# Kernel tuning notes

Measured on AMD Instinct MI355X. Metric: run time of the kernel, lower is better.

Reference implementation:

```python
import jax, jax.numpy as jnp
import numpy as np

B, L, W = 512, 16, 256


def setup_inputs() -> dict:
    key = jax.random.key(0)
    k = jax.random.split(key, 9)
    f32 = jnp.float32
    # spin configuration in {-1, +1}
    x = jax.random.randint(k[0], (B, L, L), 0, 2).astype(f32) * 2.0 - 1.0
    s = 1.0 / np.sqrt(W)
    W_ih = jax.random.normal(k[1], (3 * W, 2), f32) * s      # GRUCell input weights
    W_hh = jax.random.normal(k[2], (3 * W, W), f32) * s      # GRUCell hidden weights
    b_ih = jax.random.normal(k[3], (3 * W,), f32) * s
    b_hh = jax.random.normal(k[4], (3 * W,), f32) * s
    W_fc = jax.random.normal(k[5], (2, W), f32) * s          # fc1
    b_fc = jax.random.normal(k[6], (2,), f32) * s
    W_hcat = jax.random.normal(k[7], (W, 2 * W), f32) * (1.0 / np.sqrt(2 * W))  # intermediate_h
    W_xcat = jax.random.normal(k[8], (1, 2), f32) * 0.5      # intermediate_x
    return dict(x=x, W_ih=W_ih, W_hh=W_hh, b_ih=b_ih, b_hh=b_hh,
                W_fc=W_fc, b_fc=b_fc, W_hcat=W_hcat, W_xcat=W_xcat)


def _log_prob(x, W_ih, W_hh, b_ih, b_hh, W_fc, b_fc, W_hcat, W_xcat):
    Bsz, Ln, _ = x.shape
    Wd = W_hh.shape[1]
    mask = (1.0 + x) * 0.5                      # (1+x)/2
    Wh_l = W_hcat[:, :Wd]                       # acts on left-neighbor hidden (cat order: [left, up])
    Wh_u = W_hcat[:, Wd:]                       # acts on up-neighbor hidden

    def step(carry, xs):
        x_left, h_left = carry                  # [B], [B,W]
        x_cur, x_up, h_up, m = xs               # [B], [B], [B,W], [B]
        # intermediate_x(stack([x_left, x_up]))
        x_int = x_left * W_xcat[0, 0] + x_up * W_xcat[0, 1]
        # intermediate_h(cat([h_left, h_up]))
        h_int = h_left @ Wh_l.T + h_up @ Wh_u.T
        # embedded_x = [(x+1)/2, 1-(x+1)/2]
        p_up = (x_int + 1.0) * 0.5
        emb = jnp.stack([p_up, 1.0 - p_up], axis=1)   # [B,2]
        # torch.nn.GRUCell math (gate order: reset, update, new)
        gi = emb @ W_ih.T + b_ih
        gh = h_int @ W_hh.T + b_hh
        ir, iz, inn = jnp.split(gi, 3, axis=1)
        hr, hz, hn = jnp.split(gh, 3, axis=1)
        r = jax.nn.sigmoid(ir + hr)
        z = jax.nn.sigmoid(iz + hz)
        n = jnp.tanh(inn + r * hn)
        h_next = (1.0 - z) * n + z * h_int
        y = jax.nn.log_softmax(h_next @ W_fc.T + b_fc, axis=1)   # [B,2]
        lp = y[:, 0] * m + y[:, 1] * (1.0 - m)
        return (x_cur, h_next), (h_next, lp)

    h_prev = jnp.zeros((Ln, Bsz, Wd), x.dtype)  # hidden of row above, columns-major [L,B,W]
    x_prev = jnp.zeros((Ln, Bsz), x.dtype)      # spins of row above [L,B]
    lp_rows = []
    for i in range(Ln):                         # fixed small structural loop over rows
        x_row = x[:, i, :].T                    # [L,B]
        m_row = mask[:, i, :].T
        x_up, h_up = x_prev, h_prev
        if i % 2 == 1:                          # zigzag: odd rows scan right-to-left
            x_row, m_row = x_row[::-1], m_row[::-1]
            x_up, h_up = x_up[::-1], h_up[::-1]
        carry0 = (jnp.zeros((Bsz,), x.dtype), jnp.zeros((Bsz, Wd), x.dtype))
        _, (h_out, lp_out) = jax.lax.scan(step, carry0, (x_row, x_up, h_up, m_row))
        if i % 2 == 1:                          # restore grid (column) order
            h_out, lp_out = h_out[::-1], lp_out[::-1]
        lp_rows.append(lp_out)                  # [L,B]
        h_prev = h_out
        x_prev = x[:, i, :].T
    lp = jnp.transpose(jnp.stack(lp_rows, axis=0), (2, 0, 1))   # [B,L,L]
    lp = lp.at[:, 0, 0].set(1.0 - mask[:, 0, 0])                # first site overwrite
    return lp.sum(axis=(1, 2))


def reference(x, W_ih, W_hh, b_ih, b_hh, W_fc, b_fc, W_hcat, W_xcat):
    # z2 == 0 and reverse == False: log_prob(x) == _log_prob(x)
    return _log_prob(x, W_ih, W_hh, b_ih, b_hh, W_fc, b_fc, W_hcat, W_xcat)
```

## Files before the change

### kernel.cpp

```cpp
#include <hip/hip_runtime.h>
#include <math.h>

#define LL 16
#define WD 256
#define G3 768

#define OFF_A8  0
#define OFF_B8  32768
#define OFF_SRB 81920
#define OFF_SRA 82688
#define OFF_GA  82944
#define OFF_GBI 83712

__device__ __forceinline__ int sdot4(unsigned a, unsigned b, int acc) {
#if __has_builtin(__builtin_amdgcn_sdot4)
    return __builtin_amdgcn_sdot4((int)a, (int)b, acc, false);
#else
    int s = acc;
    #pragma unroll
    for (int r = 0; r < 4; ++r)
        s += (int)(signed char)(a >> (8 * r)) * (int)(signed char)(b >> (8 * r));
    return s;
#endif
}
__device__ __forceinline__ float fsig(float v) { return 1.f / (1.f + __expf(-v)); }
__device__ __forceinline__ float ftanh_(float v) {
    v = fminf(fmaxf(v, -15.f), 15.f);
    float e = __expf(-2.f * v);
    return (1.f - e) / (1.f + e);
}
__device__ __forceinline__ int clampi8(int q) {
    return q > 127 ? 127 : (q < -127 ? -127 : q);
}

__global__ __launch_bounds__(64)
void gru2d_prep1(const float* __restrict__ W_hh, const float* __restrict__ W_hcat,
                 float* __restrict__ ws) {
    int row = blockIdx.x, lane = threadIdx.x;
    float s = 0.f;
    if (row < 768) {
        for (int k = lane; k < 256; k += 64) s = fmaxf(s, fabsf(W_hh[row * 256 + k]));
    } else {
        int r = row - 768;
        for (int k = lane; k < 512; k += 64) s = fmaxf(s, fabsf(W_hcat[r * 512 + k]));
    }
    #pragma unroll
    for (int o = 32; o > 0; o >>= 1) s = fmaxf(s, __shfl_down(s, o));
    if (lane == 0) {
        float sc = (s > 0.f) ? s * (1.f / 127.f) : 1.f;
        if (row < 768) ws[OFF_SRB + row] = sc;
        else           ws[OFF_SRA + (row - 768)] = sc;
    }
}

__global__ __launch_bounds__(256)
void gru2d_prep2(const float* __restrict__ W_ih, const float* __restrict__ W_hh,
                 const float* __restrict__ b_ih, const float* __restrict__ W_hcat,
                 float* __restrict__ ws) {
    unsigned* __restrict__ wsu = (unsigned*)ws;
    int m = blockIdx.x * 256 + threadIdx.x;
    if (m < 32768) {
        int g4 = m >> 11, t = (m >> 2) & 511, r = m & 3;
        int j = g4 * 4 + r;
        int w = t & 255, ch = t >> 8;
        float inv = 1.f / ws[OFF_SRA + w];
        int base = w * 512 + ch * 256 + 4 * j;
        unsigned pk = 0;
        #pragma unroll
        for (int bb = 0; bb < 4; ++bb) {
            int qv = clampi8(__float2int_rn(W_hcat[base + bb] * inv));
            pk |= ((unsigned)(qv & 255)) << (8 * bb);
        }
        wsu[OFF_A8 + m] = pk;
    } else if (m < 81920) {
        int mm = m - 32768;
        int g4 = mm >> 11, t = (mm >> 2) & 511, rr = mm & 3;
        int ql = g4 * 4 + rr;
        int gate = ql >> 5, q = ql & 31;
        int v = t >> 6, l = t & 63;
        int wB_ = v * 32 + (l & 31), chB = l >> 5;
        int row = gate * 256 + wB_;
        float inv = 1.f / ws[OFF_SRB + row];
        int kb = row * 256 + chB * 128 + 4 * q;
        unsigned pk = 0;
        #pragma unroll
        for (int bb = 0; bb < 4; ++bb) {
            int qv = clampi8(__float2int_rn(W_hh[kb + bb] * inv));
            pk |= ((unsigned)(qv & 255)) << (8 * bb);
        }
        wsu[OFF_B8 + mm] = pk;
    } else if (m < 82688) {
        int e = m - 81920;
        float w0 = W_ih[2 * e], w1 = W_ih[2 * e + 1];
        ws[OFF_GA + e] = w0 - w1;
        ws[OFF_GBI + e] = w1 + b_ih[e];
    }
}

__global__ __launch_bounds__(512, 2)
void gru2d_main(const float* __restrict__ x, const float* __restrict__ b_hh,
                const float* __restrict__ W_fc, const float* __restrict__ b_fc,
                const float* __restrict__ W_xcat, const float* __restrict__ ws,
                float* __restrict__ out) {
    __shared__ __attribute__((aligned(16))) unsigned h8[2][64];
    __shared__ __attribute__((aligned(16))) unsigned hp8[2][LL][64];
    __shared__ float hs8[2][8];
    __shared__ float hps8[2][LL][8];
    __shared__ __attribute__((aligned(16))) float pA[2][2][256];
    __shared__ __attribute__((aligned(16))) float shint[2][256];
    __shared__ __attribute__((aligned(16))) unsigned hint8q[2][64];
    __shared__ float dqs[2][4];
    __shared__ float fcp[2][2][8];
    __shared__ float sx[2][256];

    const int tid = threadIdx.x;
    const int w = tid & 255;
    const int ch = tid >> 8;
    const int v = tid >> 6, l = tid & 63;
    const int lr = l & 31, sub = l >> 5;
    const int wB_ = (v << 5) + lr;
    const int b0 = blockIdx.x * 2;
    const unsigned* __restrict__ wsu = (const unsigned*)ws;

    unsigned wA8[64], wB8[96];
    #pragma unroll
    for (int g = 0; g < 16; ++g) {
        uint4 q = ((const uint4*)(wsu + OFF_A8))[g * 512 + tid];
        wA8[4*g] = q.x; wA8[4*g+1] = q.y; wA8[4*g+2] = q.z; wA8[4*g+3] = q.w;
    }
    #pragma unroll
    for (int g = 0; g < 24; ++g) {
        uint4 q = ((const uint4*)(wsu + OFF_B8))[g * 512 + tid];
        wB8[4*g] = q.x; wB8[4*g+1] = q.y; wB8[4*g+2] = q.z; wB8[4*g+3] = q.w;
    }

    const float ascale = ws[OFF_SRA + w];
    float bA[3], bBi[3], bbh[3], bsr[3];
    #pragma unroll
    for (int g = 0; g < 3; ++g) {
        bA[g]  = ws[OFF_GA + (g << 8) + wB_];
        bBi[g] = ws[OFF_GBI + (g << 8) + wB_];
        bbh[g] = b_hh[(g << 8) + wB_];
        bsr[g] = ws[OFF_SRB + (g << 8) + wB_];
    }
    const float wfc0 = W_fc[wB_], wfc1 = W_fc[256 + wB_];
    sx[ch][w] = x[(b0 + ch) * 256 + w];
    {
        unsigned* hp = (unsigned*)hp8;
        #pragma unroll
        for (int g = 0; g < 4; ++g) hp[g * 512 + tid] = 0u;
        if (tid < 256) ((float*)hps8)[tid] = 0.f;
    }
    const float xc0 = W_xcat[0], xc1 = W_xcat[1];
    const float bf0 = b_fc[0], bf1 = b_fc[1];
    float lp_acc = 0.f;
    __syncthreads();

    for (int i = 0; i < LL; ++i) {
        const int odd = i & 1;
        const int dir = odd ? -1 : 1;
        const int c0g = odd ? (LL - 1) : 0;
        for (int t = 0; t < LL; ++t) {
            const int col = c0g + dir * t;
            const int sidx = (i << 4) + t;

            #pragma unroll
            for (int g = 0; g < 16; ++g)
                asm volatile("" : "+v"(wA8[4*g]), "+v"(wA8[4*g+1]), "+v"(wA8[4*g+2]), "+v"(wA8[4*g+3]));
            #pragma unroll
            for (int g = 0; g < 24; ++g)
                asm volatile("" : "+v"(wB8[4*g]), "+v"(wB8[4*g+1]), "+v"(wB8[4*g+2]), "+v"(wB8[4*g+3]));

            {
                const uint4* Hb0;
                const uint4* Hb1;
                const float* sc0;
                const float* sc1;
                if (ch == 0) {
                    Hb0 = (const uint4*)h8[0];       Hb1 = (const uint4*)h8[1];
                    sc0 = hs8[0];                     sc1 = hs8[1];
                } else {
                    Hb0 = (const uint4*)hp8[0][col]; Hb1 = (const uint4*)hp8[1][col];
                    sc0 = hps8[0][col];               sc1 = hps8[1][col];
                }
                float fa0 = 0.f, fa1 = 0.f;
                if (!(ch == 0 && t == 0)) {
                    #pragma unroll
                    for (int c = 0; c < 8; ++c) {
                        uint4 u0a = Hb0[2*c], u0b = Hb0[2*c+1];
                        uint4 u1a = Hb1[2*c], u1b = Hb1[2*c+1];
                        int a0 = 0, a1 = 0;
                        const int kk = c << 3;
                        a0 = sdot4(wA8[kk],   u0a.x, a0); a0 = sdot4(wA8[kk+1], u0a.y, a0);
                        a0 = sdot4(wA8[kk+2], u0a.z, a0); a0 = sdot4(wA8[kk+3], u0a.w, a0);
                        a0 = sdot4(wA8[kk+4], u0b.x, a0); a0 = sdot4(wA8[kk+5], u0b.y, a0);
                        a0 = sdot4(wA8[kk+6], u0b.z, a0); a0 = sdot4(wA8[kk+7], u0b.w, a0);
                        a1 = sdot4(wA8[kk],   u1a.x, a1); a1 = sdot4(wA8[kk+1], u1a.y, a1);
                        a1 = sdot4(wA8[kk+2], u1a.z, a1); a1 = sdot4(wA8[kk+3], u1a.w, a1);
                        a1 = sdot4(wA8[kk+4], u1b.x, a1); a1 = sdot4(wA8[kk+5], u1b.y, a1);
                        a1 = sdot4(wA8[kk+6], u1b.z, a1); a1 = sdot4(wA8[kk+7], u1b.w, a1);
                        fa0 += (float)a0 * sc0[c];
                        fa1 += (float)a1 * sc1[c];
                    }
                    fa0 *= ascale;
                    fa1 *= ascale;
                }
                pA[ch][0][w] = fa0;
                pA[ch][1][w] = fa1;
            }
            __syncthreads();

            {
                float hi = pA[0][ch][w] + pA[1][ch][w];
                shint[ch][w] = hi;
                float am = fabsf(hi);
                #pragma unroll
                for (int o = 1; o < 64; o <<= 1) am = fmaxf(am, __shfl_xor(am, o));
                float qsc = 127.f / fmaxf(am, 1e-20f);
                int q = clampi8(__float2int_rn(hi * qsc));
                ((unsigned char*)hint8q)[(ch << 8) + w] = (unsigned char)(q & 255);
                if ((w & 63) == 0) dqs[ch][w >> 6] = am * (1.f / 127.f);

                if (w == 0 && sidx > 0) {
                    int ps = sidx - 1, pi2 = ps >> 4, pt2 = ps & 15;
                    int pcol = (pi2 & 1) ? (15 - pt2) : pt2;
                    float l0 = bf0, l1 = bf1;
                    #pragma unroll
                    for (int vv = 0; vv < 8; ++vv) { l0 += fcp[ch][0][vv]; l1 += fcp[ch][1][vv]; }
                    float mx = fmaxf(l0, l1);
                    float lse = mx + logf(__expf(l0 - mx) + __expf(l1 - mx));
                    float xcur = sx[ch][(pi2 << 4) + pcol];
                    float mm = (1.f + xcur) * 0.5f;
                    float lp = (l0 - lse) * mm + (l1 - lse) * (1.f - mm);
                    if (pi2 == 0 && pcol == 0) lp = 1.f - mm;
                    lp_acc += lp;
                }
            }
            __syncthreads();

            {
                const uint4* hq0 = ((const uint4*)hint8q) + (sub << 3);
                const uint4* hq1 = ((const uint4*)hint8q) + 16 + (sub << 3);
                int ra0=0,ra1=0,za0=0,za1=0,na0=0,na1=0;
                int rb0=0,rb1=0,zb0=0,zb1=0,nb0=0,nb1=0;
                #pragma unroll
                for (int gg = 0; gg < 4; ++gg) {
                    uint4 u0 = hq0[gg], u1 = hq1[gg];
                    const int k = gg << 2;
                    ra0 = sdot4(wB8[k],      u0.x, ra0); ra0 = sdot4(wB8[k+1],    u0.y, ra0);
                    ra0 = sdot4(wB8[k+2],    u0.z, ra0); ra0 = sdot4(wB8[k+3],    u0.w, ra0);
                    za0 = sdot4(wB8[32+k],   u0.x, za0); za0 = sdot4(wB8[32+k+1], u0.y, za0);
                    za0 = sdot4(wB8[32+k+2], u0.z, za0); za0 = sdot4(wB8[32+k+3], u0.w, za0);
                    na0 = sdot4(wB8[64+k],   u0.x, na0); na0 = sdot4(wB8[64+k+1], u0.y, na0);
                    na0 = sdot4(wB8[64+k+2], u0.z, na0); na0 = sdot4(wB8[64+k+3], u0.w, na0);
                    ra1 = sdot4(wB8[k],      u1.x, ra1); ra1 = sdot4(wB8[k+1],    u1.y, ra1);
                    ra1 = sdot4(wB8[k+2],    u1.z, ra1); ra1 = sdot4(wB8[k+3],    u1.w, ra1);
                    za1 = sdot4(wB8[32+k],   u1.x, za1); za1 = sdot4(wB8[32+k+1], u1.y, za1);
                    za1 = sdot4(wB8[32+k+2], u1.z, za1); za1 = sdot4(wB8[32+k+3], u1.w, za1);
                    na1 = sdot4(wB8[64+k],   u1.x, na1); na1 = sdot4(wB8[64+k+1], u1.y, na1);
                    na1 = sdot4(wB8[64+k+2], u1.z, na1); na1 = sdot4(wB8[64+k+3], u1.w, na1);
                }
                #pragma unroll
                for (int gg = 4; gg < 8; ++gg) {
                    uint4 u0 = hq0[gg], u1 = hq1[gg];
                    const int k = gg << 2;
                    rb0 = sdot4(wB8[k],      u0.x, rb0); rb0 = sdot4(wB8[k+1],    u0.y, rb0);
                    rb0 = sdot4(wB8[k+2],    u0.z, rb0); rb0 = sdot4(wB8[k+3],    u0.w, rb0);
                    zb0 = sdot4(wB8[32+k],   u0.x, zb0); zb0 = sdot4(wB8[32+k+1], u0.y, zb0);
                    zb0 = sdot4(wB8[32+k+2], u0.z, zb0); zb0 = sdot4(wB8[32+k+3], u0.w, zb0);
                    nb0 = sdot4(wB8[64+k],   u0.x, nb0); nb0 = sdot4(wB8[64+k+1], u0.y, nb0);
                    nb0 = sdot4(wB8[64+k+2], u0.z, nb0); nb0 = sdot4(wB8[64+k+3], u0.w, nb0);
                    rb1 = sdot4(wB8[k],      u1.x, rb1); rb1 = sdot4(wB8[k+1],    u1.y, rb1);
                    rb1 = sdot4(wB8[k+2],    u1.z, rb1); rb1 = sdot4(wB8[k+3],    u1.w, rb1);
                    zb1 = sdot4(wB8[32+k],   u1.x, zb1); zb1 = sdot4(wB8[32+k+1], u1.y, zb1);
                    zb1 = sdot4(wB8[32+k+2], u1.z, zb1); zb1 = sdot4(wB8[32+k+3], u1.w, zb1);
                    nb1 = sdot4(wB8[64+k],   u1.x, nb1); nb1 = sdot4(wB8[64+k+1], u1.y, nb1);
                    nb1 = sdot4(wB8[64+k+2], u1.z, nb1); nb1 = sdot4(wB8[64+k+3], u1.w, nb1);
                }
                const float d00 = dqs[0][2*sub], d01 = dqs[0][2*sub+1];
                const float d10 = dqs[1][2*sub], d11 = dqs[1][2*sub+1];
                float gr0 = (float)ra0 * d00 + (float)rb0 * d01;
                float gz0 = (float)za0 * d00 + (float)zb0 * d01;
                float gn0 = (float)na0 * d00 + (float)nb0 * d01;
                float gr1 = (float)ra1 * d10 + (float)rb1 * d11;
                float gz1 = (float)za1 * d10 + (float)zb1 * d11;
                float gn1 = (float)na1 * d10 + (float)nb1 * d11;
                gr0 += __shfl_xor(gr0, 32); gz0 += __shfl_xor(gz0, 32); gn0 += __shfl_xor(gn0, 32);
                gr1 += __shfl_xor(gr1, 32); gz1 += __shfl_xor(gz1, 32); gn1 += __shfl_xor(gn1, 32);

                const int bsel = sub;
                float GR = (bsel ? gr1 : gr0) * bsr[0];
                float GZ = (bsel ? gz1 : gz0) * bsr[1];
                float GN = (bsel ? gn1 : gn0) * bsr[2];
                float HI = shint[bsel][wB_];
                float xl = (t == 0) ? 0.f : sx[bsel][(i << 4) + col - dir];
                float xu = (i == 0) ? 0.f : sx[bsel][((i - 1) << 4) + col];
                float pu = (xl * xc0 + xu * xc1 + 1.f) * 0.5f;
                float rr_ = fsig(bA[0] * pu + bBi[0] + GR + bbh[0]);
                float zz = fsig(bA[1] * pu + bBi[1] + GZ + bbh[1]);
                float nn = ftanh_(bA[2] * pu + bBi[2] + rr_ * (GN + bbh[2]));
                float hn = (1.f - zz) * nn + zz * HI;

                float am = fabsf(hn);
                #pragma unroll
                for (int o = 1; o < 32; o <<= 1) am = fmaxf(am, __shfl_xor(am, o));
                float qs = 127.f / fmaxf(am, 1e-20f);
                unsigned q = (unsigned)(clampi8(__float2int_rn(hn * qs)) & 255);
                unsigned q1 = __shfl_down(q, 1);
                unsigned q2 = __shfl_down(q, 2);
                unsigned q3 = __shfl_down(q, 3);
                if ((lr & 3) == 0) {
                    unsigned pk = q | (q1 << 8) | (q2 << 16) | (q3 << 24);
                    int idx = (v << 3) + (lr >> 2);
                    h8[bsel][idx] = pk;
                    hp8[bsel][col][idx] = pk;
                }
                if (lr == 0) {
                    float hsc = am * (1.f / 127.f);
                    hs8[bsel][v] = hsc;
                    hps8[bsel][col][v] = hsc;
                }

                float s0 = hn * wfc0, s1 = hn * wfc1;
                #pragma unroll
                for (int o = 1; o < 32; o <<= 1) {
                    s0 += __shfl_xor(s0, o);
                    s1 += __shfl_xor(s1, o);
                }
                if (lr == 0) { fcp[bsel][0][v] = s0; fcp[bsel][1][v] = s1; }
            }
            __syncthreads();
        }
    }

    if (w == 0) {
        float l0 = bf0, l1 = bf1;
        #pragma unroll
        for (int vv = 0; vv < 8; ++vv) { l0 += fcp[ch][0][vv]; l1 += fcp[ch][1][vv]; }
        float mx = fmaxf(l0, l1);
        float lse = mx + logf(__expf(l0 - mx) + __expf(l1 - mx));
        float xcur = sx[ch][15 * 16 + 0];
        float mm = (1.f + xcur) * 0.5f;
        lp_acc += (l0 - lse) * mm + (l1 - lse) * (1.f - mm);
        out[b0 + ch] = lp_acc;
    }
}

extern "C" void kernel_launch(void* const* d_in, const int* in_sizes, int n_in,
                              void* d_out, int out_size, void* d_ws, size_t ws_size,
                              hipStream_t stream) {
    const float* x      = (const float*)d_in[0];
    const float* W_ih   = (const float*)d_in[1];
    const float* W_hh   = (const float*)d_in[2];
    const float* b_ih   = (const float*)d_in[3];
    const float* b_hh   = (const float*)d_in[4];
    const float* W_fc   = (const float*)d_in[5];
    const float* b_fc   = (const float*)d_in[6];
    const float* W_hcat = (const float*)d_in[7];
    const float* W_xcat = (const float*)d_in[8];
    float* out = (float*)d_out;
    float* ws  = (float*)d_ws;

    gru2d_prep1<<<1024, 64, 0, stream>>>(W_hh, W_hcat, ws);
    gru2d_prep2<<<323, 256, 0, stream>>>(W_ih, W_hh, b_ih, W_hcat, ws);
    gru2d_main<<<256, 512, 0, stream>>>(x, b_hh, W_fc, b_fc, W_xcat, ws, out);
}
```

Measured before the change: 946.0 us.

## Remap first matvec to wave-local K split and drop one barrier per step

The intermediate-h matvec now splits K across half-waves (lanes 0-31 left, 32-63 up), so each wave holds the same output columns as the GRU gate stage. Partial sums combine with a cross-lane shuffle instead of going through shared memory, which removes the pA/shint buffers and one __syncthreads per step. Quantized hidden state is written as bytes directly instead of being packed with shuffles. The weight prep layout and the dequant-scale granularity change to match, which adds more per-chunk scale multiplies in the second matvec.

Result: faster. 899.4 us (-4.9%).

```diff
diff --git a/kernel.cpp b/kernel.cpp
--- a/kernel.cpp
+++ b/kernel.cpp
@@ -62,9 +62,10 @@
     if (m < 32768) {
         int g4 = m >> 11, t = (m >> 2) & 511, r = m & 3;
         int j = g4 * 4 + r;
-        int w = t & 255, ch = t >> 8;
+        int v = t >> 6, l = t & 63;
+        int w = v * 32 + (l & 31), kh = l >> 5;
         float inv = 1.f / ws[OFF_SRA + w];
-        int base = w * 512 + ch * 256 + 4 * j;
+        int base = w * 512 + kh * 256 + 4 * j;
         unsigned pk = 0;
         #pragma unroll
         for (int bb = 0; bb < 4; ++bb) {
@@ -78,10 +79,10 @@
         int ql = g4 * 4 + rr;
         int gate = ql >> 5, q = ql & 31;
         int v = t >> 6, l = t & 63;
-        int wB_ = v * 32 + (l & 31), chB = l >> 5;
-        int row = gate * 256 + wB_;
+        int w = v * 32 + (l & 31), kh = l >> 5;
+        int row = gate * 256 + w;
         float inv = 1.f / ws[OFF_SRB + row];
-        int kb = row * 256 + chB * 128 + 4 * q;
+        int kb = row * 256 + kh * 128 + 4 * q;
         unsigned pk = 0;
         #pragma unroll
         for (int bb = 0; bb < 4; ++bb) {
@@ -106,19 +107,15 @@
     __shared__ __attribute__((aligned(16))) unsigned hp8[2][LL][64];
     __shared__ float hs8[2][8];
     __shared__ float hps8[2][LL][8];
-    __shared__ __attribute__((aligned(16))) float pA[2][2][256];
-    __shared__ __attribute__((aligned(16))) float shint[2][256];
     __shared__ __attribute__((aligned(16))) unsigned hint8q[2][64];
-    __shared__ float dqs[2][4];
+    __shared__ float dqs[2][8];
     __shared__ float fcp[2][2][8];
     __shared__ float sx[2][256];
 
     const int tid = threadIdx.x;
-    const int w = tid & 255;
-    const int ch = tid >> 8;
     const int v = tid >> 6, l = tid & 63;
     const int lr = l & 31, sub = l >> 5;
-    const int wB_ = (v << 5) + lr;
+    const int w = (v << 5) + lr;
     const int b0 = blockIdx.x * 2;
     const unsigned* __restrict__ wsu = (const unsigned*)ws;
 
@@ -138,13 +135,13 @@
     float bA[3], bBi[3], bbh[3], bsr[3];
     #pragma unroll
     for (int g = 0; g < 3; ++g) {
-        bA[g]  = ws[OFF_GA + (g << 8) + wB_];
-        bBi[g] = ws[OFF_GBI + (g << 8) + wB_];
-        bbh[g] = b_hh[(g << 8) + wB_];
-        bsr[g] = ws[OFF_SRB + (g << 8) + wB_];
-    }
-    const float wfc0 = W_fc[wB_], wfc1 = W_fc[256 + wB_];
-    sx[ch][w] = x[(b0 + ch) * 256 + w];
+        bA[g]  = ws[OFF_GA + (g << 8) + w];
+        bBi[g] = ws[OFF_GBI + (g << 8) + w];
+        bbh[g] = b_hh[(g << 8) + w];
+        bsr[g] = ws[OFF_SRB + (g << 8) + w];
+    }
+    const float wfc0 = W_fc[w], wfc1 = W_fc[256 + w];
+    sx[tid >> 8][tid & 255] = x[(b0 + (tid >> 8)) * 256 + (tid & 255)];
     {
         unsigned* hp = (unsigned*)hp8;
         #pragma unroll
@@ -171,120 +168,103 @@
             for (int g = 0; g < 24; ++g)
                 asm volatile("" : "+v"(wB8[4*g]), "+v"(wB8[4*g+1]), "+v"(wB8[4*g+2]), "+v"(wB8[4*g+3]));
 
+            if ((tid == 0 || tid == 256) && sidx > 0) {
+                const int b = tid >> 8;
+                int ps = sidx - 1, pi2 = ps >> 4, pt2 = ps & 15;
+                int pcol = (pi2 & 1) ? (15 - pt2) : pt2;
+                float l0 = bf0, l1 = bf1;
+                #pragma unroll
+                for (int vv = 0; vv < 8; ++vv) { l0 += fcp[b][0][vv]; l1 += fcp[b][1][vv]; }
+                float mx = fmaxf(l0, l1);
+                float lse = mx + logf(__expf(l0 - mx) + __expf(l1 - mx));
+                float xcur = sx[b][(pi2 << 4) + pcol];
+                float mm = (1.f + xcur) * 0.5f;
+                float lp = (l0 - lse) * mm + (l1 - lse) * (1.f - mm);
+                if (pi2 == 0 && pcol == 0) lp = 1.f - mm;
+                lp_acc += lp;
+            }
+
+            float hi_sel;
             {
-                const uint4* Hb0;
-                const uint4* Hb1;
-                const float* sc0;
-                const float* sc1;
-                if (ch == 0) {
-                    Hb0 = (const uint4*)h8[0];       Hb1 = (const uint4*)h8[1];
-                    sc0 = hs8[0];                     sc1 = hs8[1];
-                } else {
-                    Hb0 = (const uint4*)hp8[0][col]; Hb1 = (const uint4*)hp8[1][col];
-                    sc0 = hps8[0][col];               sc1 = hps8[1][col];
-                }
                 float fa0 = 0.f, fa1 = 0.f;
-                if (!(ch == 0 && t == 0)) {
+                if (!(sub == 0 && t == 0)) {
+                    const uint4* H0 = sub ? (const uint4*)hp8[0][col] : (const uint4*)h8[0];
+                    const uint4* H1 = sub ? (const uint4*)hp8[1][col] : (const uint4*)h8[1];
+                    const float* s0p = sub ? hps8[0][col] : hs8[0];
+                    const float* s1p = sub ? hps8[1][col] : hs8[1];
                     #pragma unroll
                     for (int c = 0; c < 8; ++c) {
-                        uint4 u0a = Hb0[2*c], u0b = Hb0[2*c+1];
-                        uint4 u1a = Hb1[2*c], u1b = Hb1[2*c+1];
+                        uint4 ua0 = H0[2*c], ub0 = H0[2*c+1];
+                        uint4 ua1 = H1[2*c], ub1 = H1[2*c+1];
+                        const int kk = c << 3;
                         int a0 = 0, a1 = 0;
-                        const int kk = c << 3;
-                        a0 = sdot4(wA8[kk],   u0a.x, a0); a0 = sdot4(wA8[kk+1], u0a.y, a0);
-                        a0 = sdot4(wA8[kk+2], u0a.z, a0); a0 = sdot4(wA8[kk+3], u0a.w, a0);
-                        a0 = sdot4(wA8[kk+4], u0b.x, a0); a0 = sdot4(wA8[kk+5], u0b.y, a0);
-                        a0 = sdot4(wA8[kk+6], u0b.z, a0); a0 = sdot4(wA8[kk+7], u0b.w, a0);
-                        a1 = sdot4(wA8[kk],   u1a.x, a1); a1 = sdot4(wA8[kk+1], u1a.y, a1);
-                        a1 = sdot4(wA8[kk+2], u1a.z, a1); a1 = sdot4(wA8[kk+3], u1a.w, a1);
-                        a1 = sdot4(wA8[kk+4], u1b.x, a1); a1 = sdot4(wA8[kk+5], u1b.y, a1);
-                        a1 = sdot4(wA8[kk+6], u1b.z, a1); a1 = sdot4(wA8[kk+7], u1b.w, a1);
-                        fa0 += (float)a0 * sc0[c];
-                        fa1 += (float)a1 * sc1[c];
+                        a0 = sdot4(wA8[kk],   ua0.x, a0); a0 = sdot4(wA8[kk+1], ua0.y, a0);
+                        a0 = sdot4(wA8[kk+2], ua0.z, a0); a0 = sdot4(wA8[kk+3], ua0.w, a0);
+                        a0 = sdot4(wA8[kk+4], ub0.x, a0); a0 = sdot4(wA8[kk+5], ub0.y, a0);
+                        a0 = sdot4(wA8[kk+6], ub0.z, a0); a0 = sdot4(wA8[kk+7], ub0.w, a0);
+                        a1 = sdot4(wA8[kk],   ua1.x, a1); a1 = sdot4(wA8[kk+1], ua1.y, a1);
+                        a1 = sdot4(wA8[kk+2], ua1.z, a1); a1 = sdot4(wA8[kk+3], ua1.w, a1);
+                        a1 = sdot4(wA8[kk+4], ub1.x, a1); a1 = sdot4(wA8[kk+5], ub1.y, a1);
+                        a1 = sdot4(wA8[kk+6], ub1.z, a1); a1 = sdot4(wA8[kk+7], ub1.w, a1);
+                        fa0 += (float)a0 * s0p[c];
+                        fa1 += (float)a1 * s1p[c];
                     }
                     fa0 *= ascale;
                     fa1 *= ascale;
                 }
-                pA[ch][0][w] = fa0;
-                pA[ch][1][w] = fa1;
-            }
-            __syncthreads();
-
-            {
-                float hi = pA[0][ch][w] + pA[1][ch][w];
-                shint[ch][w] = hi;
-                float am = fabsf(hi);
-                #pragma unroll
-                for (int o = 1; o < 64; o <<= 1) am = fmaxf(am, __shfl_xor(am, o));
+                fa0 += __shfl_xor(fa0, 32);
+                fa1 += __shfl_xor(fa1, 32);
+                hi_sel = sub ? fa1 : fa0;
+                float am = fabsf(hi_sel);
+                #pragma unroll
+                for (int o = 1; o < 32; o <<= 1) am = fmaxf(am, __shfl_xor(am, o));
                 float qsc = 127.f / fmaxf(am, 1e-20f);
-                int q = clampi8(__float2int_rn(hi * qsc));
-                ((unsigned char*)hint8q)[(ch << 8) + w] = (unsigned char)(q & 255);
-                if ((w & 63) == 0) dqs[ch][w >> 6] = am * (1.f / 127.f);
-
-                if (w == 0 && sidx > 0) {
-                    int ps = sidx - 1, pi2 = ps >> 4, pt2 = ps & 15;
-                    int pcol = (pi2 & 1) ? (15 - pt2) : pt2;
-                    float l0 = bf0, l1 = bf1;
-                    #pragma unroll
-                    for (int vv = 0; vv < 8; ++vv) { l0 += fcp[ch][0][vv]; l1 += fcp[ch][1][vv]; }
-                    float mx = fmaxf(l0, l1);
-                    float lse = mx + logf(__expf(l0 - mx) + __expf(l1 - mx));
-                    float xcur = sx[ch][(pi2 << 4) + pcol];
-                    float mm = (1.f + xcur) * 0.5f;
-                    float lp = (l0 - lse) * mm + (l1 - lse) * (1.f - mm);
-                    if (pi2 == 0 && pcol == 0) lp = 1.f - mm;
-                    lp_acc += lp;
-                }
+                int q = clampi8(__float2int_rn(hi_sel * qsc));
+                ((unsigned char*)hint8q)[(sub << 8) + w] = (unsigned char)(q & 255);
+                if (lr == 0) dqs[sub][v] = am * (1.f / 127.f);
             }
             __syncthreads();
 
             {
                 const uint4* hq0 = ((const uint4*)hint8q) + (sub << 3);
                 const uint4* hq1 = ((const uint4*)hint8q) + 16 + (sub << 3);
-                int ra0=0,ra1=0,za0=0,za1=0,na0=0,na1=0;
-                int rb0=0,rb1=0,zb0=0,zb1=0,nb0=0,nb1=0;
-                #pragma unroll
-                for (int gg = 0; gg < 4; ++gg) {
-                    uint4 u0 = hq0[gg], u1 = hq1[gg];
-                    const int k = gg << 2;
-                    ra0 = sdot4(wB8[k],      u0.x, ra0); ra0 = sdot4(wB8[k+1],    u0.y, ra0);
-                    ra0 = sdot4(wB8[k+2],    u0.z, ra0); ra0 = sdot4(wB8[k+3],    u0.w, ra0);
-                    za0 = sdot4(wB8[32+k],   u0.x, za0); za0 = sdot4(wB8[32+k+1], u0.y, za0);
-                    za0 = sdot4(wB8[32+k+2], u0.z, za0); za0 = sdot4(wB8[32+k+3], u0.w, za0);
-                    na0 = sdot4(wB8[64+k],   u0.x, na0); na0 = sdot4(wB8[64+k+1], u0.y, na0);
-                    na0 = sdot4(wB8[64+k+2], u0.z, na0); na0 = sdot4(wB8[64+k+3], u0.w, na0);
-                    ra1 = sdot4(wB8[k],      u1.x, ra1); ra1 = sdot4(wB8[k+1],    u1.y, ra1);
-                    ra1 = sdot4(wB8[k+2],    u1.z, ra1); ra1 = sdot4(wB8[k+3],    u1.w, ra1);
-                    za1 = sdot4(wB8[32+k],   u1.x, za1); za1 = sdot4(wB8[32+k+1], u1.y, za1);
-                    za1 = sdot4(wB8[32+k+2], u1.z, za1); za1 = sdot4(wB8[32+k+3], u1.w, za1);
-                    na1 = sdot4(wB8[64+k],   u1.x, na1); na1 = sdot4(wB8[64+k+1], u1.y, na1);
-                    na1 = sdot4(wB8[64+k+2], u1.z, na1); na1 = sdot4(wB8[64+k+3], u1.w, na1);
+                const float* dq0 = &dqs[0][sub << 2];
+                const float* dq1 = &dqs[1][sub << 2];
+                float gr0 = 0.f, gz0 = 0.f, gn0 = 0.f, gr1 = 0.f, gz1 = 0.f, gn1 = 0.f;
+                #pragma unroll
+                for (int c2 = 0; c2 < 4; ++c2) {
+                    uint4 u0a = hq0[2*c2], u0b = hq0[2*c2+1];
+                    uint4 u1a = hq1[2*c2], u1b = hq1[2*c2+1];
+                    const int k = c2 << 3;
+                    int r0 = 0, z0 = 0, n0 = 0, r1 = 0, z1 = 0, n1 = 0;
+                    r0 = sdot4(wB8[k],      u0a.x, r0); r0 = sdot4(wB8[k+1],    u0a.y, r0);
+                    r0 = sdot4(wB8[k+2],    u0a.z, r0); r0 = sdot4(wB8[k+3],    u0a.w, r0);
+                    r0 = sdot4(wB8[k+4],    u0b.x, r0); r0 = sdot4(wB8[k+5],    u0b.y, r0);
+                    r0 = sdot4(wB8[k+6],    u0b.z, r0); r0 = sdot4(wB8[k+7],    u0b.w, r0);
+                    z0 = sdot4(wB8[32+k],   u0a.x, z0); z0 = sdot4(wB8[32+k+1], u0a.y, z0);
+                    z0 = sdot4(wB8[32+k+2], u0a.z, z0); z0 = sdot4(wB8[32+k+3], u0a.w, z0);
+                    z0 = sdot4(wB8[32+k+4], u0b.x, z0); z0 = sdot4(wB8[32+k+5], u0b.y, z0);
+                    z0 = sdot4(wB8[32+k+6], u0b.z, z0); z0 = sdot4(wB8[32+k+7], u0b.w, z0);
+                    n0 = sdot4(wB8[64+k],   u0a.x, n0); n0 = sdot4(wB8[64+k+1], u0a.y, n0);
+                    n0 = sdot4(wB8[64+k+2], u0a.z, n0); n0 = sdot4(wB8[64+k+3], u0a.w, n0);
+                    n0 = sdot4(wB8[64+k+4], u0b.x, n0); n0 = sdot4(wB8[64+k+5], u0b.y, n0);
+                    n0 = sdot4(wB8[64+k+6], u0b.z, n0); n0 = sdot4(wB8[64+k+7], u0b.w, n0);
+                    r1 = sdot4(wB8[k],      u1a.x, r1); r1 = sdot4(wB8[k+1],    u1a.y, r1);
+                    r1 = sdot4(wB8[k+2],    u1a.z, r1); r1 = sdot4(wB8[k+3],    u1a.w, r1);
+                    r1 = sdot4(wB8[k+4],    u1b.x, r1); r1 = sdot4(wB8[k+5],    u1b.y, r1);
+                    r1 = sdot4(wB8[k+6],    u1b.z, r1); r1 = sdot4(wB8[k+7],    u1b.w, r1);
+                    z1 = sdot4(wB8[32+k],   u1a.x, z1); z1 = sdot4(wB8[32+k+1], u1a.y, z1);
+                    z1 = sdot4(wB8[32+k+2], u1a.z, z1); z1 = sdot4(wB8[32+k+3], u1a.w, z1);
+                    z1 = sdot4(wB8[32+k+4], u1b.x, z1); z1 = sdot4(wB8[32+k+5], u1b.y, z1);
+                    z1 = sdot4(wB8[32+k+6], u1b.z, z1); z1 = sdot4(wB8[32+k+7], u1b.w, z1);
+                    n1 = sdot4(wB8[64+k],   u1a.x, n1); n1 = sdot4(wB8[64+k+1], u1a.y, n1);
+                    n1 = sdot4(wB8[64+k+2], u1a.z, n1); n1 = sdot4(wB8[64+k+3], u1a.w, n1);
+                    n1 = sdot4(wB8[64+k+4], u1b.x, n1); n1 = sdot4(wB8[64+k+5], u1b.y, n1);
+                    n1 = sdot4(wB8[64+k+6], u1b.z, n1); n1 = sdot4(wB8[64+k+7], u1b.w, n1);
+                    const float d0 = dq0[c2], d1 = dq1[c2];
+                    gr0 += (float)r0 * d0; gz0 += (float)z0 * d0; gn0 += (float)n0 * d0;
+                    gr1 += (float)r1 * d1; gz1 += (float)z1 * d1; gn1 += (float)n1 * d1;
                 }
-                #pragma unroll
-                for (int gg = 4; gg < 8; ++gg) {
-                    uint4 u0 = hq0[gg], u1 = hq1[gg];
-                    const int k = gg << 2;
-                    rb0 = sdot4(wB8[k],      u0.x, rb0); rb0 = sdot4(wB8[k+1],    u0.y, rb0);
-                    rb0 = sdot4(wB8[k+2],    u0.z, rb0); rb0 = sdot4(wB8[k+3],    u0.w, rb0);
-                    zb0 = sdot4(wB8[32+k],   u0.x, zb0); zb0 = sdot4(wB8[32+k+1], u0.y, zb0);
-                    zb0 = sdot4(wB8[32+k+2], u0.z, zb0); zb0 = sdot4(wB8[32+k+3], u0.w, zb0);
-                    nb0 = sdot4(wB8[64+k],   u0.x, nb0); nb0 = sdot4(wB8[64+k+1], u0.y, nb0);
-                    nb0 = sdot4(wB8[64+k+2], u0.z, nb0); nb0 = sdot4(wB8[64+k+3], u0.w, nb0);
-                    rb1 = sdot4(wB8[k],      u1.x, rb1); rb1 = sdot4(wB8[k+1],    u1.y, rb1);
-                    rb1 = sdot4(wB8[k+2],    u1.z, rb1); rb1 = sdot4(wB8[k+3],    u1.w, rb1);
-                    zb1 = sdot4(wB8[32+k],   u1.x, zb1); zb1 = sdot4(wB8[32+k+1], u1.y, zb1);
-                    zb1 = sdot4(wB8[32+k+2], u1.z, zb1); zb1 = sdot4(wB8[32+k+3], u1.w, zb1);
-                    nb1 = sdot4(wB8[64+k],   u1.x, nb1); nb1 = sdot4(wB8[64+k+1], u1.y, nb1);
-                    nb1 = sdot4(wB8[64+k+2], u1.z, nb1); nb1 = sdot4(wB8[64+k+3], u1.w, nb1);
-                }
-                const float d00 = dqs[0][2*sub], d01 = dqs[0][2*sub+1];
-                const float d10 = dqs[1][2*sub], d11 = dqs[1][2*sub+1];
-                float gr0 = (float)ra0 * d00 + (float)rb0 * d01;
-                float gz0 = (float)za0 * d00 + (float)zb0 * d01;
-                float gn0 = (float)na0 * d00 + (float)nb0 * d01;
-                float gr1 = (float)ra1 * d10 + (float)rb1 * d11;
-                float gz1 = (float)za1 * d10 + (float)zb1 * d11;
-                float gn1 = (float)na1 * d10 + (float)nb1 * d11;
                 gr0 += __shfl_xor(gr0, 32); gz0 += __shfl_xor(gz0, 32); gn0 += __shfl_xor(gn0, 32);
                 gr1 += __shfl_xor(gr1, 32); gz1 += __shfl_xor(gz1, 32); gn1 += __shfl_xor(gn1, 32);
 
@@ -292,33 +272,25 @@
                 float GR = (bsel ? gr1 : gr0) * bsr[0];
                 float GZ = (bsel ? gz1 : gz0) * bsr[1];
                 float GN = (bsel ? gn1 : gn0) * bsr[2];
-                float HI = shint[bsel][wB_];
                 float xl = (t == 0) ? 0.f : sx[bsel][(i << 4) + col - dir];
                 float xu = (i == 0) ? 0.f : sx[bsel][((i - 1) << 4) + col];
                 float pu = (xl * xc0 + xu * xc1 + 1.f) * 0.5f;
                 float rr_ = fsig(bA[0] * pu + bBi[0] + GR + bbh[0]);
                 float zz = fsig(bA[1] * pu + bBi[1] + GZ + bbh[1]);
                 float nn = ftanh_(bA[2] * pu + bBi[2] + rr_ * (GN + bbh[2]));
-                float hn = (1.f - zz) * nn + zz * HI;
+                float hn = (1.f - zz) * nn + zz * hi_sel;
 
                 float am = fabsf(hn);
                 #pragma unroll
                 for (int o = 1; o < 32; o <<= 1) am = fmaxf(am, __shfl_xor(am, o));
                 float qs = 127.f / fmaxf(am, 1e-20f);
-                unsigned q = (unsigned)(clampi8(__float2int_rn(hn * qs)) & 255);
-                unsigned q1 = __shfl_down(q, 1);
-                unsigned q2 = __shfl_down(q, 2);
-                unsigned q3 = __shfl_down(q, 3);
-                if ((lr & 3) == 0) {
-                    unsigned pk = q | (q1 << 8) | (q2 << 16) | (q3 << 24);
-                    int idx = (v << 3) + (lr >> 2);
-                    h8[bsel][idx] = pk;
-                    hp8[bsel][col][idx] = pk;
-                }
+                int q = clampi8(__float2int_rn(hn * qs));
+                ((unsigned char*)h8)[(sub << 8) + w] = (unsigned char)(q & 255);
+                ((unsigned char*)hp8)[(sub << 12) + (col << 8) + w] = (unsigned char)(q & 255);
                 if (lr == 0) {
                     float hsc = am * (1.f / 127.f);
-                    hs8[bsel][v] = hsc;
-                    hps8[bsel][col][v] = hsc;
+                    hs8[sub][v] = hsc;
+                    hps8[sub][col][v] = hsc;
                 }
 
                 float s0 = hn * wfc0, s1 = hn * wfc1;
@@ -327,22 +299,23 @@
                     s0 += __shfl_xor(s0, o);
                     s1 += __shfl_xor(s1, o);
                 }
-                if (lr == 0) { fcp[bsel][0][v] = s0; fcp[bsel][1][v] = s1; }
+                if (lr == 0) { fcp[sub][0][v] = s0; fcp[sub][1][v] = s1; }
             }
             __syncthreads();
         }
     }
 
-    if (w == 0) {
+    if (tid == 0 || tid == 256) {
+        const int b = tid >> 8;
         float l0 = bf0, l1 = bf1;
         #pragma unroll
-        for (int vv = 0; vv < 8; ++vv) { l0 += fcp[ch][0][vv]; l1 += fcp[ch][1][vv]; }
+        for (int vv = 0; vv < 8; ++vv) { l0 += fcp[b][0][vv]; l1 += fcp[b][1][vv]; }
         float mx = fmaxf(l0, l1);
         float lse = mx + logf(__expf(l0 - mx) + __expf(l1 - mx));
-        float xcur = sx[ch][15 * 16 + 0];
+        float xcur = sx[b][15 * 16 + 0];
         float mm = (1.f + xcur) * 0.5f;
         lp_acc += (l0 - lse) * mm + (l1 - lse) * (1.f - mm);
-        out[b0 + ch] = lp_acc;
+        out[b0 + b] = lp_acc;
     }
 }
 
```
